# Kernel optimization log

Measured on AMD Instinct MI355X. Metric: run time of the kernel, lower is better.

The kernel has to match this reference:

```python
import jax, jax.numpy as jnp
import numpy as np

INPUT, HIDDEN = 40, 250
B, T = 256, 512


def lstm_layer(x_seq, W_ih, W_hh, b_ih, b_hh):
    """x_seq: [B,T,D_in] -> [B,T,H]. PyTorch gate order: i,f,g,o."""
    # Precompute input contribution with one big GEMM: [B,T,4H]
    xg = jnp.einsum('btd,gd->btg', x_seq, W_ih) + b_ih + b_hh
    xg_t = jnp.transpose(xg, (1, 0, 2))  # [T,B,4H]
    H = W_hh.shape[1]
    h0 = jnp.zeros((x_seq.shape[0], H), dtype=x_seq.dtype)
    c0 = jnp.zeros_like(h0)

    def step(carry, g_in):
        h, c = carry
        g = g_in + h @ W_hh.T  # [B,4H]
        i = jax.nn.sigmoid(g[:, :H])
        f = jax.nn.sigmoid(g[:, H:2 * H])
        gg = jnp.tanh(g[:, 2 * H:3 * H])
        o = jax.nn.sigmoid(g[:, 3 * H:])
        c = f * c + i * gg
        h = o * jnp.tanh(c)
        return (h, c), h

    _, hs = jax.lax.scan(step, (h0, c0), xg_t)  # hs: [T,B,H]
    return jnp.transpose(hs, (1, 0, 2))


def setup_inputs() -> dict:
    key = jax.random.key(0)
    ks = jax.random.split(key, 12)
    s_in = 1.0 / np.sqrt(HIDDEN)  # PyTorch LSTM init scale
    u = lambda k, shape: jax.random.uniform(k, shape, jnp.float32, -s_in, s_in)
    return {
        'x': jax.random.normal(ks[0], (B, T, INPUT), jnp.float32),
        'W_ih0': u(ks[1], (4 * HIDDEN, INPUT)),
        'W_hh0': u(ks[2], (4 * HIDDEN, HIDDEN)),
        'b_ih0': u(ks[3], (4 * HIDDEN,)),
        'b_hh0': u(ks[4], (4 * HIDDEN,)),
        'W_ih1': u(ks[5], (4 * HIDDEN, HIDDEN)),
        'W_hh1': u(ks[6], (4 * HIDDEN, HIDDEN)),
        'b_ih1': u(ks[7], (4 * HIDDEN,)),
        'b_hh1': u(ks[8], (4 * HIDDEN,)),
        'W_lin': u(ks[9], (1, HIDDEN)),
        'b_lin': u(ks[10], (1,)),
    }


def reference(x, W_ih0, W_hh0, b_ih0, b_hh0, W_ih1, W_hh1, b_ih1, b_hh1, W_lin, b_lin):
    h1 = lstm_layer(x, W_ih0, W_hh0, b_ih0, b_hh0)   # [B,T,H]
    h2 = lstm_layer(h1, W_ih1, W_hh1, b_ih1, b_hh1)  # [B,T,H]
    y = jnp.einsum('bth,oh->bto', h2, W_lin) + b_lin  # [B,T,1]
    return jax.nn.sigmoid(y)
```

## Files before the change

### kernel.cpp

```cpp
#include <hip/hip_runtime.h>
#include <cstdint>

#define B_TOT 256
#define T_LEN 512
#define NX    40
#define NH    250
#define HP    256
#define XP    64
#define K0    (XP + HP)
#define K1    (HP + HP)
#define MB    32
#define NU    16
#define NR    64
#define RING  8
#define LDSK  520
#define SLOTS 16
#define NFLAG (2 * 8 * 16 * SLOTS)
#define RSTEP (B_TOT * HP / 2)
#define XCD_AT(w) ((w) * SLOTS + 8)
#define BAR_IDX 9
#define GETREG_XCC 63508

typedef __attribute__((ext_vector_type(8))) short short8;
typedef __attribute__((ext_vector_type(4))) float float4v;

__device__ __forceinline__ unsigned short f2bf(float f) {
  unsigned u = __float_as_uint(f);
  u += 0x7FFFu + ((u >> 16) & 1u);
  return (unsigned short)(u >> 16);
}
__device__ __forceinline__ float bf2f(unsigned short h) {
  return __uint_as_float(((unsigned)h) << 16);
}
__device__ __forceinline__ float sigm(float x) { return 1.0f / (1.0f + __expf(-x)); }
__device__ __forceinline__ float tanh_f(float x) {
  float e = __expf(-2.0f * fabsf(x));
  float t = (1.0f - e) / (1.0f + e);
  return copysignf(t, x);
}
__device__ __forceinline__ unsigned ld_lic(const unsigned* p) {
  return __hip_atomic_load(p, __ATOMIC_RELAXED, __HIP_MEMORY_SCOPE_AGENT);
}
__device__ __forceinline__ void inv_l1() {
  asm volatile("buffer_inv\n\ts_waitcnt vmcnt(0)" ::: "memory");
  __builtin_amdgcn_sched_barrier(0);
}
template <bool FAST>
__device__ __forceinline__ unsigned ldh(const unsigned* p) {
  if (FAST) return *p;
  return ld_lic(p);
}
template <bool FAST>
__device__ __forceinline__ void sth(unsigned* p, unsigned v) {
  if (FAST) *p = v;
  else __hip_atomic_store(p, v, __ATOMIC_RELAXED, __HIP_MEMORY_SCOPE_AGENT);
}

template <int KSTEPS, int LAYER, bool FAST>
__device__ __forceinline__ void run_layer(
    int tid, int gg, int b0, int u0,
    const float* __restrict__ x, float* __restrict__ out, float blinv,
    unsigned short* __restrict__ h1bc, unsigned short* __restrict__ h2bc,
    int* __restrict__ c0s, int* __restrict__ c1s, int* __restrict__ mys,
    unsigned short (*WL)[LDSK], unsigned short (*inA)[LDSK],
    float (*gbuf)[NR + 4], float* biasS, float* wlinS) {
  const int lane = tid & 63, wv = tid >> 6;
  const int quad = lane >> 4, l15 = lane & 15;
  const int Mt = wv & 1, Np = wv >> 1;
  const int gb = b0 >> 5;
  const int irow = tid >> 3, icol = tid & 7;

  short8 wfrag[2][KSTEPS];
#pragma unroll
  for (int ks = 0; ks < KSTEPS; ++ks) {
#pragma unroll
    for (int i = 0; i < 2; ++i)
      wfrag[i][ks] = *(const short8*)&WL[Np * 32 + i * 16 + l15][ks * 32 + quad * 8];
  }

  float4v b4A = *(const float4v*)&biasS[Np * 32 + quad * 4];
  float4v b4B = *(const float4v*)&biasS[Np * 32 + 16 + quad * 4];

  float xr[10];
  if (LAYER == 0 && tid < 128) {
    int b = tid >> 2, c = tid & 3;
    const float* xp0 = x + ((size_t)(b0 + b) * T_LEN + 0) * NX + c * 10;
#pragma unroll
    for (int j = 0; j < 10; ++j) xr[j] = xp0[j];
  }

  float cA = 0.f, cB = 0.f;

#pragma unroll 1
  for (int t = 0; t < T_LEN; ++t) {
    if (wv == 0 && lane < 32) {
      const int* sl = ((lane < 16) ? c0s : c1s) + (lane & 15) * SLOTS;
      int thr;
      if (LAYER == 0) thr = (lane < 16) ? t : (t - RING + 1);
      else            thr = (lane < 16) ? (t + 1) : t;
      while (__hip_atomic_load(sl, __ATOMIC_RELAXED, __HIP_MEMORY_SCOPE_AGENT) < thr) {
        __builtin_amdgcn_s_sleep(1);
      }
    }
    __syncthreads();
    if (FAST && (LAYER == 1 || t > 0)) inv_l1();

    if (LAYER == 0) {
      if (t > 0) {
        const unsigned* s1 = (const unsigned*)h1bc +
            ((size_t)((t - 1) & (RING - 1)) * RSTEP + (size_t)gb * 4096);
        unsigned v[16];
#pragma unroll
        for (int k = 0; k < 16; ++k) v[k] = ldh<FAST>(s1 + tid + k * 256);
#pragma unroll
        for (int k = 0; k < 16; ++k)
          ((unsigned*)&inA[irow][0])[32 + k * 8 + icol] = v[k];
      }
      if (tid < 128) {
        int b = tid >> 2, c = tid & 3;
#pragma unroll
        for (int j = 0; j < 10; ++j) inA[b][c * 10 + j] = f2bf(xr[j]);
      }
    } else {
      const unsigned* s1 = (const unsigned*)h1bc +
          ((size_t)(t & (RING - 1)) * RSTEP + (size_t)gb * 4096);
      unsigned va[16], vb[16];
#pragma unroll
      for (int k = 0; k < 16; ++k) va[k] = ldh<FAST>(s1 + tid + k * 256);
      if (t > 0) {
        const unsigned* s2 = (const unsigned*)h2bc +
            ((size_t)((t - 1) & (RING - 1)) * RSTEP + (size_t)gb * 4096);
#pragma unroll
        for (int k = 0; k < 16; ++k) vb[k] = ldh<FAST>(s2 + tid + k * 256);
      }
#pragma unroll
      for (int k = 0; k < 16; ++k) {
        unsigned* row = (unsigned*)&inA[irow][0];
        row[k * 8 + icol] = va[k];
        if (t > 0) row[128 + k * 8 + icol] = vb[k];
      }
    }
    __syncthreads();

    if (LAYER == 0 && tid < 128 && t + 1 < T_LEN) {
      int b = tid >> 2, c = tid & 3;
      const float* xp = x + ((size_t)(b0 + b) * T_LEN + (size_t)(t + 1)) * NX + c * 10;
#pragma unroll
      for (int j = 0; j < 10; ++j) xr[j] = xp[j];
    }

    float4v acc0 = {0.f, 0.f, 0.f, 0.f};
    float4v acc1 = {0.f, 0.f, 0.f, 0.f};
#pragma unroll
    for (int ks = 0; ks < KSTEPS; ++ks) {
      short8 a = *(const short8*)&inA[Mt * 16 + l15][ks * 32 + quad * 8];
      acc0 = __builtin_amdgcn_mfma_f32_16x16x32_bf16(wfrag[0][ks], a, acc0, 0, 0, 0);
      acc1 = __builtin_amdgcn_mfma_f32_16x16x32_bf16(wfrag[1][ks], a, acc1, 0, 0, 0);
    }

    float hA, hB;
    {
      float i0 = sigm(acc0[0] + b4A[0]);
      float f0 = sigm(acc0[1] + b4A[1]);
      float g0 = tanh_f(acc0[2] + b4A[2]);
      float o0 = sigm(acc0[3] + b4A[3]);
      cA = f0 * cA + i0 * g0;
      hA = o0 * tanh_f(cA);
      float i1 = sigm(acc1[0] + b4B[0]);
      float f1 = sigm(acc1[1] + b4B[1]);
      float g1 = tanh_f(acc1[2] + b4B[2]);
      float o1 = sigm(acc1[3] + b4B[3]);
      cB = f1 * cB + i1 * g1;
      hB = o1 * tanh_f(cB);
    }
    {
      float hA2 = __shfl_xor(hA, 16);
      float hB2 = __shfl_xor(hB, 16);
      if ((quad & 1) == 0) {
        unsigned dwA = (unsigned)f2bf(hA) | ((unsigned)f2bf(hA2) << 16);
        unsigned dwB = (unsigned)f2bf(hB) | ((unsigned)f2bf(hB2) << 16);
        unsigned* dst = (unsigned*)(LAYER ? h2bc : h1bc);
        size_t base = (size_t)(t & (RING - 1)) * RSTEP + (size_t)gb * 4096 +
                      (size_t)gg * 256 + (size_t)(Mt * 16 + l15) * 8;
        sth<FAST>(dst + base + Np * 4 + (quad >> 1), dwA);
        sth<FAST>(dst + base + Np * 4 + 2 + (quad >> 1), dwB);
      }
    }

    __syncthreads();
    if (tid == 0)
      sth<FAST>((unsigned*)mys, (unsigned)(t + 1));

    if (LAYER == 1 && t > 0 && tid < 16) {
      int eb2 = 2 * gg + (tid >> 3), uc = tid & 7;
      float sum = 0.f;
#pragma unroll
      for (int j = 0; j < 4; ++j) {
        short8 hvv = *(const short8*)&inA[eb2][HP + uc * 32 + j * 8];
#pragma unroll
        for (int e = 0; e < 8; ++e)
          sum += bf2f((unsigned short)hvv[e]) * wlinS[uc * 32 + j * 8 + e];
      }
      sum += __shfl_xor(sum, 1);
      sum += __shfl_xor(sum, 2);
      sum += __shfl_xor(sum, 4);
      if ((tid & 7) == 0)
        out[(size_t)(b0 + eb2) * T_LEN + (t - 1)] = sigm(sum + blinv);
    }
  }

  if (LAYER == 1) {
    if (wv == 0 && lane < 16) {
      const int* sl = c1s + lane * SLOTS;
      while (__hip_atomic_load(sl, __ATOMIC_RELAXED, __HIP_MEMORY_SCOPE_AGENT) < T_LEN) {
        __builtin_amdgcn_s_sleep(1);
      }
    }
    __syncthreads();
    if (FAST) inv_l1();
    if (tid < 16) {
      int eb2 = 2 * gg + (tid >> 3), uc = tid & 7;
      const unsigned* base = (const unsigned*)h2bc +
          ((size_t)(511 & (RING - 1)) * RSTEP + (size_t)gb * 4096);
      float sum = 0.f;
#pragma unroll
      for (int g = 0; g < 2; ++g) {
        const unsigned* src = base + (size_t)(2 * uc + g) * 256 + eb2 * 8;
#pragma unroll
        for (int j = 0; j < 8; ++j) {
          unsigned dw = ldh<FAST>(src + j);
          sum += bf2f((unsigned short)(dw & 0xFFFFu)) * wlinS[uc * 32 + g * 16 + 2 * j];
          sum += bf2f((unsigned short)(dw >> 16)) * wlinS[uc * 32 + g * 16 + 2 * j + 1];
        }
      }
      sum += __shfl_xor(sum, 1);
      sum += __shfl_xor(sum, 2);
      sum += __shfl_xor(sum, 4);
      if ((tid & 7) == 0)
        out[(size_t)(b0 + eb2) * T_LEN + 511] = sigm(sum + blinv);
    }
  }
}

extern "C" __global__ void __launch_bounds__(256, 1) lstm_persist(
    const float* __restrict__ x,
    const float* __restrict__ Wih0, const float* __restrict__ Whh0,
    const float* __restrict__ bih0, const float* __restrict__ bhh0,
    const float* __restrict__ Wih1, const float* __restrict__ Whh1,
    const float* __restrict__ bih1, const float* __restrict__ bhh1,
    const float* __restrict__ Wlin, const float* __restrict__ blin,
    float* __restrict__ out,
    unsigned short* __restrict__ h1bc, unsigned short* __restrict__ h2bc,
    int* __restrict__ cnt) {
  __shared__ unsigned short WL[NR][LDSK];
  __shared__ unsigned short inA[MB][LDSK];
  __shared__ float gbuf[MB][NR + 4];
  __shared__ float biasS[NR];
  __shared__ float wlinS[HP];

  const int tid = threadIdx.x;
  const int wg = blockIdx.x;

  const unsigned xcc = ((unsigned)__builtin_amdgcn_s_getreg(GETREG_XCC)) & 15u;
  if (tid == 0) {
    __hip_atomic_store(cnt + XCD_AT(wg), (int)xcc, __ATOMIC_RELAXED,
                       __HIP_MEMORY_SCOPE_AGENT);
    __hip_atomic_fetch_add(cnt + BAR_IDX, 1, __ATOMIC_ACQ_REL,
                           __HIP_MEMORY_SCOPE_AGENT);
    while (__hip_atomic_load(cnt + BAR_IDX, __ATOMIC_ACQUIRE,
                             __HIP_MEMORY_SCOPE_AGENT) < 256)
      __builtin_amdgcn_s_sleep(8);
  }
  __syncthreads();
  int* sx = (int*)&gbuf[0][0];
  sx[tid] = __hip_atomic_load(cnt + XCD_AT(tid), __ATOMIC_RELAXED,
                              __HIP_MEMORY_SCOPE_AGENT);
  __syncthreads();
  const int myv = sx[wg];
  int rank = 0;
  unsigned long long hist = 0;
  bool ok = true;
  for (int j = 0; j < 256; ++j) {
    int v = sx[j];
    if ((unsigned)v > 7u) { ok = false; v = 0; }
    hist += 1ull << (v * 8);
    if (v == myv && j < wg) rank++;
  }
  ok = ok && (hist == 0x2020202020202020ull);
  __syncthreads();

  int layer, gb, gg;
  if (ok) { gb = myv;       layer = rank >> 4;    gg = rank & 15; }
  else    { layer = wg >> 7; gb = (wg >> 4) & 7;  gg = wg & 15;   }
  const int b0 = gb * MB, u0 = gg * NU;

  {
    const float* Wih = layer ? Wih1 : Wih0;
    const float* Whh = layer ? Whh1 : Whh0;
    const float* bi = layer ? bih1 : bih0;
    const float* bh = layer ? bhh1 : bhh0;
    const int K = layer ? K1 : K0;
    const int xw = layer ? NH : NX;
    const int xofs = layer ? HP : XP;
    int r = tid >> 2, c = tid & 3;
    int lu = r >> 2, g = r & 3, ug = u0 + lu;
    int row = g * NH + ug;
    int kq = K >> 2;
    for (int k = c * kq; k < (c + 1) * kq; ++k) {
      float v = 0.f;
      if (ug < NH) {
        if (k < xw) v = Wih[(size_t)row * xw + k];
        else if (k >= xofs && k < xofs + NH) v = Whh[(size_t)row * NH + (k - xofs)];
      }
      WL[r][k] = f2bf(v);
    }
    if (tid < NR) {
      int lu2 = tid >> 2, g2 = tid & 3, ug2 = u0 + lu2;
      biasS[tid] = (ug2 < NH) ? (bi[g2 * NH + ug2] + bh[g2 * NH + ug2]) : 0.f;
    }
    if (tid < HP) wlinS[tid] = (tid < NH) ? Wlin[tid] : 0.f;
    for (int i = tid; i < MB * LDSK; i += 256) ((unsigned short*)inA)[i] = 0;
  }
  __syncthreads();

  float blinv = blin[0];
  int* c0s = cnt + gb * 16 * SLOTS;
  int* c1s = cnt + (8 + gb) * 16 * SLOTS;
  int* mys = (layer ? c1s : c0s) + gg * SLOTS;

  if (ok) {
    if (layer == 0)
      run_layer<K0 / 32, 0, true>(tid, gg, b0, u0, x, out, blinv, h1bc, h2bc,
                                  c0s, c1s, mys, WL, inA, gbuf, biasS, wlinS);
    else
      run_layer<K1 / 32, 1, true>(tid, gg, b0, u0, x, out, blinv, h1bc, h2bc,
                                  c0s, c1s, mys, WL, inA, gbuf, biasS, wlinS);
  } else {
    if (layer == 0)
      run_layer<K0 / 32, 0, false>(tid, gg, b0, u0, x, out, blinv, h1bc, h2bc,
                                   c0s, c1s, mys, WL, inA, gbuf, biasS, wlinS);
    else
      run_layer<K1 / 32, 1, false>(tid, gg, b0, u0, x, out, blinv, h1bc, h2bc,
                                   c0s, c1s, mys, WL, inA, gbuf, biasS, wlinS);
  }
}

extern "C" __global__ void prep_zero(int* cnt) {
  int i = blockIdx.x * 256 + threadIdx.x;
  if (i < NFLAG)
    __hip_atomic_store(cnt + i, 0, __ATOMIC_RELAXED, __HIP_MEMORY_SCOPE_AGENT);
}

extern "C" void kernel_launch(void* const* d_in, const int* in_sizes, int n_in,
                              void* d_out, int out_size, void* d_ws, size_t ws_size,
                              hipStream_t stream) {
  const float* x    = (const float*)d_in[0];
  const float* Wih0 = (const float*)d_in[1];
  const float* Whh0 = (const float*)d_in[2];
  const float* bih0 = (const float*)d_in[3];
  const float* bhh0 = (const float*)d_in[4];
  const float* Wih1 = (const float*)d_in[5];
  const float* Whh1 = (const float*)d_in[6];
  const float* bih1 = (const float*)d_in[7];
  const float* bhh1 = (const float*)d_in[8];
  const float* Wlin = (const float*)d_in[9];
  const float* blin = (const float*)d_in[10];
  float* out = (float*)d_out;

  unsigned short* h1bc = (unsigned short*)d_ws;
  unsigned short* h2bc = h1bc + (size_t)RING * B_TOT * HP;
  int* cnt = (int*)((char*)d_ws + 2u * (size_t)RING * B_TOT * HP * sizeof(unsigned short));

  hipLaunchKernelGGL(prep_zero, dim3(16), dim3(256), 0, stream, cnt);

  void* args[] = {&x, &Wih0, &Whh0, &bih0, &bhh0, &Wih1, &Whh1, &bih1, &bhh1,
                  &Wlin, &blin, &out, &h1bc, &h2bc, &cnt};
  hipLaunchCooperativeKernel((void*)lstm_persist, dim3(256), dim3(256), args, 0u, stream);
}
```

Before: 1.189 ms.

## Replace per-step block barriers with per-wave flags and double-buffered LDS input

Each wave now publishes its own progress flag after draining its global stores, instead of the whole block syncing and thread 0 publishing one flag. Every wave polls all 64 wave flags of its own and the other layer directly, so the spin-wait plus __syncthreads at the top of each step and the barrier before the flag store are gone. The LDS input tile is double-buffered so the next step's writes cannot race with readers of the current step, and the x prefetch for layer 0 moves earlier to overlap with the h loads. In exchange there are more flag polls per wave and twice the LDS for the input tile, and correctness now relies on per-wave drain ordering.

```diff
diff --git a/kernel.cpp b/kernel.cpp
--- a/kernel.cpp
+++ b/kernel.cpp
@@ -14,11 +14,11 @@
 #define NR    64
 #define RING  8
 #define LDSK  520
-#define SLOTS 16
-#define NFLAG (2 * 8 * 16 * SLOTS)
+#define NFLAG 4096
+#define GSTRIDE 256
 #define RSTEP (B_TOT * HP / 2)
-#define XCD_AT(w) ((w) * SLOTS + 8)
-#define BAR_IDX 9
+#define XCD_AT(w) ((w) * 4 + 1)
+#define BAR_IDX 3
 #define GETREG_XCC 63508
 
 typedef __attribute__((ext_vector_type(8))) short short8;
@@ -38,11 +38,18 @@
   float t = (1.0f - e) / (1.0f + e);
   return copysignf(t, x);
 }
+__device__ __forceinline__ int ld_flag(const int* p) {
+  return __hip_atomic_load(p, __ATOMIC_RELAXED, __HIP_MEMORY_SCOPE_AGENT);
+}
 __device__ __forceinline__ unsigned ld_lic(const unsigned* p) {
   return __hip_atomic_load(p, __ATOMIC_RELAXED, __HIP_MEMORY_SCOPE_AGENT);
 }
 __device__ __forceinline__ void inv_l1() {
   asm volatile("buffer_inv\n\ts_waitcnt vmcnt(0)" ::: "memory");
+  __builtin_amdgcn_sched_barrier(0);
+}
+__device__ __forceinline__ void drain_vm() {
+  asm volatile("s_waitcnt vmcnt(0)" ::: "memory");
   __builtin_amdgcn_sched_barrier(0);
 }
 template <bool FAST>
@@ -61,15 +68,19 @@
     int tid, int gg, int b0, int u0,
     const float* __restrict__ x, float* __restrict__ out, float blinv,
     unsigned short* __restrict__ h1bc, unsigned short* __restrict__ h2bc,
-    int* __restrict__ c0s, int* __restrict__ c1s, int* __restrict__ mys,
-    unsigned short (*WL)[LDSK], unsigned short (*inA)[LDSK],
-    float (*gbuf)[NR + 4], float* biasS, float* wlinS) {
+    int* __restrict__ c0s, int* __restrict__ c1s,
+    unsigned short (*WL)[LDSK], unsigned short (*inA2)[LDSK],
+    float* biasS, float* wlinS) {
   const int lane = tid & 63, wv = tid >> 6;
   const int quad = lane >> 4, l15 = lane & 15;
   const int Mt = wv & 1, Np = wv >> 1;
   const int gb = b0 >> 5;
   const int irow = tid >> 3, icol = tid & 7;
 
+  const int* ownS = (LAYER ? c1s : c0s) + lane * 4;
+  const int* othS = (LAYER ? c0s : c1s) + lane * 4;
+  int* mysub = (LAYER ? c1s : c0s) + (wv * 16 + gg) * 4;
+
   short8 wfrag[2][KSTEPS];
 #pragma unroll
   for (int ks = 0; ks < KSTEPS; ++ks) {
@@ -93,33 +104,39 @@
 
 #pragma unroll 1
   for (int t = 0; t < T_LEN; ++t) {
-    if (wv == 0 && lane < 32) {
-      const int* sl = ((lane < 16) ? c0s : c1s) + (lane & 15) * SLOTS;
-      int thr;
-      if (LAYER == 0) thr = (lane < 16) ? t : (t - RING + 1);
-      else            thr = (lane < 16) ? (t + 1) : t;
-      while (__hip_atomic_load(sl, __ATOMIC_RELAXED, __HIP_MEMORY_SCOPE_AGENT) < thr) {
-        __builtin_amdgcn_s_sleep(1);
-      }
-    }
-    __syncthreads();
+    {
+      const int thrOwn = t;
+      const int thrOth = LAYER ? (t + 1) : (t - RING + 1);
+      while (ld_flag(ownS) < thrOwn) __builtin_amdgcn_s_sleep(1);
+      while (ld_flag(othS) < thrOth) __builtin_amdgcn_s_sleep(1);
+    }
+    if (!FAST) __syncthreads();
     if (FAST && (LAYER == 1 || t > 0)) inv_l1();
 
+    unsigned short (*inbuf)[LDSK] = inA2 + (t & 1) * MB;
+
     if (LAYER == 0) {
+      unsigned v[16];
       if (t > 0) {
         const unsigned* s1 = (const unsigned*)h1bc +
             ((size_t)((t - 1) & (RING - 1)) * RSTEP + (size_t)gb * 4096);
-        unsigned v[16];
 #pragma unroll
         for (int k = 0; k < 16; ++k) v[k] = ldh<FAST>(s1 + tid + k * 256);
-#pragma unroll
-        for (int k = 0; k < 16; ++k)
-          ((unsigned*)&inA[irow][0])[32 + k * 8 + icol] = v[k];
       }
       if (tid < 128) {
         int b = tid >> 2, c = tid & 3;
 #pragma unroll
-        for (int j = 0; j < 10; ++j) inA[b][c * 10 + j] = f2bf(xr[j]);
+        for (int j = 0; j < 10; ++j) inbuf[b][c * 10 + j] = f2bf(xr[j]);
+        if (t + 1 < T_LEN) {
+          const float* xp = x + ((size_t)(b0 + b) * T_LEN + (size_t)(t + 1)) * NX + c * 10;
+#pragma unroll
+          for (int j = 0; j < 10; ++j) xr[j] = xp[j];
+        }
+      }
+      if (t > 0) {
+#pragma unroll
+        for (int k = 0; k < 16; ++k)
+          ((unsigned*)&inbuf[irow][0])[32 + k * 8 + icol] = v[k];
       }
     } else {
       const unsigned* s1 = (const unsigned*)h1bc +
@@ -135,25 +152,18 @@
       }
 #pragma unroll
       for (int k = 0; k < 16; ++k) {
-        unsigned* row = (unsigned*)&inA[irow][0];
+        unsigned* row = (unsigned*)&inbuf[irow][0];
         row[k * 8 + icol] = va[k];
         if (t > 0) row[128 + k * 8 + icol] = vb[k];
       }
     }
     __syncthreads();
 
-    if (LAYER == 0 && tid < 128 && t + 1 < T_LEN) {
-      int b = tid >> 2, c = tid & 3;
-      const float* xp = x + ((size_t)(b0 + b) * T_LEN + (size_t)(t + 1)) * NX + c * 10;
-#pragma unroll
-      for (int j = 0; j < 10; ++j) xr[j] = xp[j];
-    }
-
     float4v acc0 = {0.f, 0.f, 0.f, 0.f};
     float4v acc1 = {0.f, 0.f, 0.f, 0.f};
 #pragma unroll
     for (int ks = 0; ks < KSTEPS; ++ks) {
-      short8 a = *(const short8*)&inA[Mt * 16 + l15][ks * 32 + quad * 8];
+      short8 a = *(const short8*)&inbuf[Mt * 16 + l15][ks * 32 + quad * 8];
       acc0 = __builtin_amdgcn_mfma_f32_16x16x32_bf16(wfrag[0][ks], a, acc0, 0, 0, 0);
       acc1 = __builtin_amdgcn_mfma_f32_16x16x32_bf16(wfrag[1][ks], a, acc1, 0, 0, 0);
     }
@@ -187,16 +197,20 @@
       }
     }
 
-    __syncthreads();
-    if (tid == 0)
-      sth<FAST>((unsigned*)mys, (unsigned)(t + 1));
+    if (FAST) {
+      drain_vm();
+      if (lane == 0) sth<true>((unsigned*)mysub, (unsigned)(t + 1));
+    } else {
+      __syncthreads();
+      if (lane == 0) sth<false>((unsigned*)mysub, (unsigned)(t + 1));
+    }
 
     if (LAYER == 1 && t > 0 && tid < 16) {
       int eb2 = 2 * gg + (tid >> 3), uc = tid & 7;
       float sum = 0.f;
 #pragma unroll
       for (int j = 0; j < 4; ++j) {
-        short8 hvv = *(const short8*)&inA[eb2][HP + uc * 32 + j * 8];
+        short8 hvv = *(const short8*)&inbuf[eb2][HP + uc * 32 + j * 8];
 #pragma unroll
         for (int e = 0; e < 8; ++e)
           sum += bf2f((unsigned short)hvv[e]) * wlinS[uc * 32 + j * 8 + e];
@@ -210,11 +224,9 @@
   }
 
   if (LAYER == 1) {
-    if (wv == 0 && lane < 16) {
-      const int* sl = c1s + lane * SLOTS;
-      while (__hip_atomic_load(sl, __ATOMIC_RELAXED, __HIP_MEMORY_SCOPE_AGENT) < T_LEN) {
-        __builtin_amdgcn_s_sleep(1);
-      }
+    if (wv == 0) {
+      const int* sl = c1s + lane * 4;
+      while (ld_flag(sl) < T_LEN) __builtin_amdgcn_s_sleep(1);
     }
     __syncthreads();
     if (FAST) inv_l1();
@@ -253,8 +265,7 @@
     unsigned short* __restrict__ h1bc, unsigned short* __restrict__ h2bc,
     int* __restrict__ cnt) {
   __shared__ unsigned short WL[NR][LDSK];
-  __shared__ unsigned short inA[MB][LDSK];
-  __shared__ float gbuf[MB][NR + 4];
+  __shared__ unsigned short inA[2 * MB][LDSK];
   __shared__ float biasS[NR];
   __shared__ float wlinS[HP];
 
@@ -272,7 +283,7 @@
       __builtin_amdgcn_s_sleep(8);
   }
   __syncthreads();
-  int* sx = (int*)&gbuf[0][0];
+  int* sx = (int*)&inA[0][0];
   sx[tid] = __hip_atomic_load(cnt + XCD_AT(tid), __ATOMIC_RELAXED,
                               __HIP_MEMORY_SCOPE_AGENT);
   __syncthreads();
@@ -319,29 +330,28 @@
       biasS[tid] = (ug2 < NH) ? (bi[g2 * NH + ug2] + bh[g2 * NH + ug2]) : 0.f;
     }
     if (tid < HP) wlinS[tid] = (tid < NH) ? Wlin[tid] : 0.f;
-    for (int i = tid; i < MB * LDSK; i += 256) ((unsigned short*)inA)[i] = 0;
+    for (int i = tid; i < 2 * MB * LDSK; i += 256) ((unsigned short*)inA)[i] = 0;
   }
   __syncthreads();
 
   float blinv = blin[0];
-  int* c0s = cnt + gb * 16 * SLOTS;
-  int* c1s = cnt + (8 + gb) * 16 * SLOTS;
-  int* mys = (layer ? c1s : c0s) + gg * SLOTS;
+  int* c0s = cnt + gb * GSTRIDE;
+  int* c1s = cnt + (8 + gb) * GSTRIDE;
 
   if (ok) {
     if (layer == 0)
       run_layer<K0 / 32, 0, true>(tid, gg, b0, u0, x, out, blinv, h1bc, h2bc,
-                                  c0s, c1s, mys, WL, inA, gbuf, biasS, wlinS);
+                                  c0s, c1s, WL, inA, biasS, wlinS);
     else
       run_layer<K1 / 32, 1, true>(tid, gg, b0, u0, x, out, blinv, h1bc, h2bc,
-                                  c0s, c1s, mys, WL, inA, gbuf, biasS, wlinS);
+                                  c0s, c1s, WL, inA, biasS, wlinS);
   } else {
     if (layer == 0)
       run_layer<K0 / 32, 0, false>(tid, gg, b0, u0, x, out, blinv, h1bc, h2bc,
-                                   c0s, c1s, mys, WL, inA, gbuf, biasS, wlinS);
+                                   c0s, c1s, WL, inA, biasS, wlinS);
     else
       run_layer<K1 / 32, 1, false>(tid, gg, b0, u0, x, out, blinv, h1bc, h2bc,
-                                   c0s, c1s, mys, WL, inA, gbuf, biasS, wlinS);
+                                   c0s, c1s, WL, inA, biasS, wlinS);
   }
 }
 
```

After: 1.313 ms. 10.5% more time.

## Load hidden-state MFMA operands directly from global into registers, bypassing LDS staging

Applied to the files above, without the earlier changes.

Each wave now loads its bf16 hidden-state B-fragments straight from the global ring buffer as 16-byte vectors laid out to match the MFMA operand format. This replaces the per-step global->LDS->register staging and the __syncthreads that followed it. Only the small x input for layer 0 still goes through a reduced LDS tile. The output projection also reads h2 from global instead of LDS. The aim is fewer LDS round trips and one fewer barrier on the serial critical path per timestep, in exchange for redundant global/L2 loads across waves and reliance on the exact write layout of the producer.

```diff
diff --git a/kernel.cpp b/kernel.cpp
--- a/kernel.cpp
+++ b/kernel.cpp
@@ -14,6 +14,7 @@
 #define NR    64
 #define RING  8
 #define LDSK  520
+#define XLDS  72
 #define SLOTS 16
 #define NFLAG (2 * 8 * 16 * SLOTS)
 #define RSTEP (B_TOT * HP / 2)
@@ -51,6 +52,14 @@
   return ld_lic(p);
 }
 template <bool FAST>
+__device__ __forceinline__ uint4 ldh4(const unsigned* p) {
+  if (FAST) return *(const uint4*)p;
+  uint4 v;
+  v.x = ld_lic(p + 0); v.y = ld_lic(p + 1);
+  v.z = ld_lic(p + 2); v.w = ld_lic(p + 3);
+  return v;
+}
+template <bool FAST>
 __device__ __forceinline__ void sth(unsigned* p, unsigned v) {
   if (FAST) *p = v;
   else __hip_atomic_store(p, v, __ATOMIC_RELAXED, __HIP_MEMORY_SCOPE_AGENT);
@@ -62,13 +71,14 @@
     const float* __restrict__ x, float* __restrict__ out, float blinv,
     unsigned short* __restrict__ h1bc, unsigned short* __restrict__ h2bc,
     int* __restrict__ c0s, int* __restrict__ c1s, int* __restrict__ mys,
-    unsigned short (*WL)[LDSK], unsigned short (*inA)[LDSK],
-    float (*gbuf)[NR + 4], float* biasS, float* wlinS) {
+    unsigned short (*WL)[LDSK], unsigned short (*xA)[XLDS],
+    float* biasS, float* wlinS) {
   const int lane = tid & 63, wv = tid >> 6;
   const int quad = lane >> 4, l15 = lane & 15;
   const int Mt = wv & 1, Np = wv >> 1;
   const int gb = b0 >> 5;
-  const int irow = tid >> 3, icol = tid & 7;
+  const int lofs = (quad >> 1) * 256 + (Mt * 16 + l15) * 8 + (quad & 1) * 4;
+  constexpr int NHF = LAYER ? KSTEPS : (KSTEPS - 2);
 
   short8 wfrag[2][KSTEPS];
 #pragma unroll
@@ -106,56 +116,69 @@
     if (FAST && (LAYER == 1 || t > 0)) inv_l1();
 
     if (LAYER == 0) {
-      if (t > 0) {
-        const unsigned* s1 = (const unsigned*)h1bc +
-            ((size_t)((t - 1) & (RING - 1)) * RSTEP + (size_t)gb * 4096);
-        unsigned v[16];
-#pragma unroll
-        for (int k = 0; k < 16; ++k) v[k] = ldh<FAST>(s1 + tid + k * 256);
-#pragma unroll
-        for (int k = 0; k < 16; ++k)
-          ((unsigned*)&inA[irow][0])[32 + k * 8 + icol] = v[k];
-      }
       if (tid < 128) {
         int b = tid >> 2, c = tid & 3;
 #pragma unroll
-        for (int j = 0; j < 10; ++j) inA[b][c * 10 + j] = f2bf(xr[j]);
+        for (int j = 0; j < 10; ++j) xA[b][c * 10 + j] = f2bf(xr[j]);
+      }
+      __syncthreads();
+      if (tid < 128 && t + 1 < T_LEN) {
+        int b = tid >> 2, c = tid & 3;
+        const float* xp = x + ((size_t)(b0 + b) * T_LEN + (size_t)(t + 1)) * NX + c * 10;
+#pragma unroll
+        for (int j = 0; j < 10; ++j) xr[j] = xp[j];
+      }
+    }
+
+    uint4 hfr[NHF];
+    if (LAYER == 0) {
+      if (t > 0) {
+        const unsigned* b1 = (const unsigned*)h1bc +
+            ((size_t)((t - 1) & (RING - 1)) * RSTEP + (size_t)gb * 4096) + lofs;
+#pragma unroll
+        for (int i = 0; i < NHF; ++i) hfr[i] = ldh4<FAST>(b1 + i * 512);
+      } else {
+#pragma unroll
+        for (int i = 0; i < NHF; ++i) hfr[i] = uint4{0, 0, 0, 0};
       }
     } else {
-      const unsigned* s1 = (const unsigned*)h1bc +
-          ((size_t)(t & (RING - 1)) * RSTEP + (size_t)gb * 4096);
-      unsigned va[16], vb[16];
-#pragma unroll
-      for (int k = 0; k < 16; ++k) va[k] = ldh<FAST>(s1 + tid + k * 256);
+      const unsigned* b1 = (const unsigned*)h1bc +
+          ((size_t)(t & (RING - 1)) * RSTEP + (size_t)gb * 4096) + lofs;
+#pragma unroll
+      for (int i = 0; i < 8; ++i) hfr[i] = ldh4<FAST>(b1 + i * 512);
       if (t > 0) {
-        const unsigned* s2 = (const unsigned*)h2bc +
-            ((size_t)((t - 1) & (RING - 1)) * RSTEP + (size_t)gb * 4096);
-#pragma unroll
-        for (int k = 0; k < 16; ++k) vb[k] = ldh<FAST>(s2 + tid + k * 256);
-      }
-#pragma unroll
-      for (int k = 0; k < 16; ++k) {
-        unsigned* row = (unsigned*)&inA[irow][0];
-        row[k * 8 + icol] = va[k];
-        if (t > 0) row[128 + k * 8 + icol] = vb[k];
-      }
-    }
-    __syncthreads();
-
-    if (LAYER == 0 && tid < 128 && t + 1 < T_LEN) {
-      int b = tid >> 2, c = tid & 3;
-      const float* xp = x + ((size_t)(b0 + b) * T_LEN + (size_t)(t + 1)) * NX + c * 10;
-#pragma unroll
-      for (int j = 0; j < 10; ++j) xr[j] = xp[j];
+        const unsigned* b2 = (const unsigned*)h2bc +
+            ((size_t)((t - 1) & (RING - 1)) * RSTEP + (size_t)gb * 4096) + lofs;
+#pragma unroll
+        for (int i = 0; i < 8; ++i) hfr[8 + i] = ldh4<FAST>(b2 + i * 512);
+      } else {
+#pragma unroll
+        for (int i = 0; i < 8; ++i) hfr[8 + i] = uint4{0, 0, 0, 0};
+      }
     }
 
     float4v acc0 = {0.f, 0.f, 0.f, 0.f};
     float4v acc1 = {0.f, 0.f, 0.f, 0.f};
-#pragma unroll
-    for (int ks = 0; ks < KSTEPS; ++ks) {
-      short8 a = *(const short8*)&inA[Mt * 16 + l15][ks * 32 + quad * 8];
-      acc0 = __builtin_amdgcn_mfma_f32_16x16x32_bf16(wfrag[0][ks], a, acc0, 0, 0, 0);
-      acc1 = __builtin_amdgcn_mfma_f32_16x16x32_bf16(wfrag[1][ks], a, acc1, 0, 0, 0);
+    if (LAYER == 0) {
+#pragma unroll
+      for (int ks = 0; ks < 2; ++ks) {
+        short8 a = *(const short8*)&xA[Mt * 16 + l15][ks * 32 + quad * 8];
+        acc0 = __builtin_amdgcn_mfma_f32_16x16x32_bf16(wfrag[0][ks], a, acc0, 0, 0, 0);
+        acc1 = __builtin_amdgcn_mfma_f32_16x16x32_bf16(wfrag[1][ks], a, acc1, 0, 0, 0);
+      }
+#pragma unroll
+      for (int i = 0; i < NHF; ++i) {
+        short8 a = *(const short8*)&hfr[i];
+        acc0 = __builtin_amdgcn_mfma_f32_16x16x32_bf16(wfrag[0][2 + i], a, acc0, 0, 0, 0);
+        acc1 = __builtin_amdgcn_mfma_f32_16x16x32_bf16(wfrag[1][2 + i], a, acc1, 0, 0, 0);
+      }
+    } else {
+#pragma unroll
+      for (int i = 0; i < KSTEPS; ++i) {
+        short8 a = *(const short8*)&hfr[i];
+        acc0 = __builtin_amdgcn_mfma_f32_16x16x32_bf16(wfrag[0][i], a, acc0, 0, 0, 0);
+        acc1 = __builtin_amdgcn_mfma_f32_16x16x32_bf16(wfrag[1][i], a, acc1, 0, 0, 0);
+      }
     }
 
     float hA, hB;
@@ -193,13 +216,18 @@
 
     if (LAYER == 1 && t > 0 && tid < 16) {
       int eb2 = 2 * gg + (tid >> 3), uc = tid & 7;
+      const unsigned* base = (const unsigned*)h2bc +
+          ((size_t)((t - 1) & (RING - 1)) * RSTEP + (size_t)gb * 4096);
       float sum = 0.f;
 #pragma unroll
-      for (int j = 0; j < 4; ++j) {
-        short8 hvv = *(const short8*)&inA[eb2][HP + uc * 32 + j * 8];
-#pragma unroll
-        for (int e = 0; e < 8; ++e)
-          sum += bf2f((unsigned short)hvv[e]) * wlinS[uc * 32 + j * 8 + e];
+      for (int g = 0; g < 2; ++g) {
+        const unsigned* src = base + (size_t)(2 * uc + g) * 256 + eb2 * 8;
+#pragma unroll
+        for (int j = 0; j < 8; ++j) {
+          unsigned dw = ldh<FAST>(src + j);
+          sum += bf2f((unsigned short)(dw & 0xFFFFu)) * wlinS[uc * 32 + g * 16 + 2 * j];
+          sum += bf2f((unsigned short)(dw >> 16)) * wlinS[uc * 32 + g * 16 + 2 * j + 1];
+        }
       }
       sum += __shfl_xor(sum, 1);
       sum += __shfl_xor(sum, 2);
@@ -253,8 +281,7 @@
     unsigned short* __restrict__ h1bc, unsigned short* __restrict__ h2bc,
     int* __restrict__ cnt) {
   __shared__ unsigned short WL[NR][LDSK];
-  __shared__ unsigned short inA[MB][LDSK];
-  __shared__ float gbuf[MB][NR + 4];
+  __shared__ unsigned short xA[MB][XLDS];
   __shared__ float biasS[NR];
   __shared__ float wlinS[HP];
 
@@ -272,7 +299,7 @@
       __builtin_amdgcn_s_sleep(8);
   }
   __syncthreads();
-  int* sx = (int*)&gbuf[0][0];
+  int* sx = (int*)&xA[0][0];
   sx[tid] = __hip_atomic_load(cnt + XCD_AT(tid), __ATOMIC_RELAXED,
                               __HIP_MEMORY_SCOPE_AGENT);
   __syncthreads();
@@ -319,7 +346,7 @@
       biasS[tid] = (ug2 < NH) ? (bi[g2 * NH + ug2] + bh[g2 * NH + ug2]) : 0.f;
     }
     if (tid < HP) wlinS[tid] = (tid < NH) ? Wlin[tid] : 0.f;
-    for (int i = tid; i < MB * LDSK; i += 256) ((unsigned short*)inA)[i] = 0;
+    for (int i = tid; i < MB * XLDS; i += 256) ((unsigned short*)xA)[i] = 0;
   }
   __syncthreads();
 
@@ -331,17 +358,17 @@
   if (ok) {
     if (layer == 0)
       run_layer<K0 / 32, 0, true>(tid, gg, b0, u0, x, out, blinv, h1bc, h2bc,
-                                  c0s, c1s, mys, WL, inA, gbuf, biasS, wlinS);
+                                  c0s, c1s, mys, WL, xA, biasS, wlinS);
     else
       run_layer<K1 / 32, 1, true>(tid, gg, b0, u0, x, out, blinv, h1bc, h2bc,
-                                  c0s, c1s, mys, WL, inA, gbuf, biasS, wlinS);
+                                  c0s, c1s, mys, WL, xA, biasS, wlinS);
   } else {
     if (layer == 0)
       run_layer<K0 / 32, 0, false>(tid, gg, b0, u0, x, out, blinv, h1bc, h2bc,
-                                   c0s, c1s, mys, WL, inA, gbuf, biasS, wlinS);
+                                   c0s, c1s, mys, WL, xA, biasS, wlinS);
     else
       run_layer<K1 / 32, 1, false>(tid, gg, b0, u0, x, out, blinv, h1bc, h2bc,
-                                   c0s, c1s, mys, WL, inA, gbuf, biasS, wlinS);
+                                   c0s, c1s, mys, WL, xA, biasS, wlinS);
   }
 }
 
```

After: 1.080 ms. 1.1x faster.
